# Optimization experiments

Measured on AMD Instinct MI355X. Metric: run time of the kernel, lower is better.

## Reference

```python
import jax, jax.numpy as jnp
import numpy as np

BATCH = 8192
IN_FEATURES = 4096
OUT_FEATURES = 4096
TT_RANK = 8
IN_MODES = (16, 16, 16)
OUT_MODES = (16, 16, 16)


def setup_inputs() -> dict:
    key = jax.random.key(0)
    ks = jax.random.split(key, 5)
    # core std ~ glorot-ish scale for TT factors
    std = 0.05
    x = jax.random.normal(ks[0], (BATCH, IN_FEATURES), dtype=jnp.float32)
    core0 = std * jax.random.normal(ks[1], (1, OUT_MODES[0], IN_MODES[0], TT_RANK), dtype=jnp.float32)
    core1 = std * jax.random.normal(ks[2], (TT_RANK, OUT_MODES[1], IN_MODES[1], TT_RANK), dtype=jnp.float32)
    core2 = std * jax.random.normal(ks[3], (TT_RANK, OUT_MODES[2], IN_MODES[2], 1), dtype=jnp.float32)
    bias = 0.001 * jnp.ones((OUT_FEATURES,), dtype=jnp.float32)
    return {"x": x, "core0": core0, "core1": core1, "core2": core2, "bias": bias}


def _tt_dense_matmul(cores, b):
    """A @ b where A (out_features x in_features) is in TT-matrix format.
    cores[k]: (r_k, o_k, i_k, r_{k+1}), r_0 = r_d = 1. b: (in_features, batch).
    Returns (out_features, batch). Mirrors t3nsor/t3f tt_dense_matmul."""
    in_dims = [c.shape[2] for c in cores]
    ranks = [c.shape[0] for c in cores] + [cores[-1].shape[3]]
    out_features = int(np.prod([c.shape[1] for c in cores]))
    data = b.T                                   # (batch, in_features)
    data = data.reshape(-1, in_dims[-1], 1)      # (batch*prod(i[:-1]), i_last, r_d=1)
    for k in range(len(cores) - 1, -1, -1):
        # core (a=r_k, i=o_k, j=i_k, b=r_{k+1}); data (r, j, b) -> (i, r, a)
        data = jnp.einsum('aijb,rjb->ira', cores[k], data)
        if k > 0:
            data = data.reshape(-1, in_dims[k - 1], ranks[k])
    return data.reshape(out_features, -1)        # (out_features, batch)


def reference(x, core0, core1, core2, bias):
    # forward: tt_dense_matmul(weight_t, x^T)^T + bias
    y = _tt_dense_matmul([core0, core1, core2], x.T)  # (out_features, batch)
    return y.T + bias                                 # (batch, out_features)
```

## Files before the change

kernel.cpp:

```cpp
#include <hip/hip_runtime.h>
#include <cstdint>


typedef __bf16 bf16x8 __attribute__((ext_vector_type(8)));
typedef float f32x4 __attribute__((ext_vector_type(4)));
typedef unsigned short u16;
typedef u16 u16x8 __attribute__((ext_vector_type(8)));

__device__ __forceinline__ u16 f2bf(float f) {
    unsigned u = __builtin_bit_cast(unsigned, f);
    u += 0x7fffu + ((u >> 16) & 1u);
    return (u16)(u >> 16);
}

__global__ void k_cvt(const float* __restrict__ x, u16* __restrict__ xb) {
    long i = (long)blockIdx.x * blockDim.x + threadIdx.x;
    const float4* p = (const float4*)x;
    float4 a = p[2 * i], b = p[2 * i + 1];
    u16x8 o;
    o[0] = f2bf(a.x); o[1] = f2bf(a.y); o[2] = f2bf(a.z); o[3] = f2bf(a.w);
    o[4] = f2bf(b.x); o[5] = f2bf(b.y); o[6] = f2bf(b.z); o[7] = f2bf(b.w);
    ((u16x8*)xb)[i] = o;
}

__global__ void k_c01(const float* __restrict__ c0, const float* __restrict__ c1,
                      float* __restrict__ c01) {
    int idx = blockIdx.x * 256 + threadIdx.x;
    int b2 = idx & 7, i1 = (idx >> 3) & 15, i0 = (idx >> 7) & 15;
    int o1 = (idx >> 11) & 15, o0 = idx >> 15;
    float s = 0.f;
#pragma unroll
    for (int b1 = 0; b1 < 8; ++b1)
        s += c0[(o0 * 16 + i0) * 8 + b1] * c1[((b1 * 16 + o1) * 16 + i1) * 8 + b2];
    c01[idx] = s;
}

__global__ void k_w(const float* __restrict__ c01, const float* __restrict__ c2,
                    u16* __restrict__ wbt) {
    int idx = blockIdx.x * 256 + threadIdx.x;
    int i2h = idx & 1;
    int i1 = (idx >> 1) & 15;
    int i0 = (idx >> 5) & 15;
    int o = idx >> 9;
    int o2 = o & 15, o1 = (o >> 4) & 15, o0 = o >> 8;
    const float* c = &c01[(((o0 * 16 + o1) * 16 + i0) * 16 + i1) * 8];
    float acc[8] = {0, 0, 0, 0, 0, 0, 0, 0};
#pragma unroll
    for (int b2 = 0; b2 < 8; ++b2) {
        float cv = c[b2];
        const float* cc = &c2[(b2 * 16 + o2) * 16 + i2h * 8];
#pragma unroll
        for (int j = 0; j < 8; ++j) acc[j] += cv * cc[j];
    }
    u16x8 ov;
#pragma unroll
    for (int j = 0; j < 8; ++j) ov[j] = f2bf(acc[j]);
    ((u16x8*)wbt)[(long)o * 512 + (i0 * 32 + i1 * 2 + i2h)] = ov;
}

#define BM 256
#define BN 256
#define BK 64
#define TILEU (BM * BK)
#define LDS_BYTES (4 * TILEU * 2)

static_assert(LDS_BYTES == 131072, "lds size");

__device__ __forceinline__ void gload_lds16(const void* g, void* l) {
    __builtin_amdgcn_global_load_lds(
        (const __attribute__((address_space(1))) unsigned*)g,
        (__attribute__((address_space(3))) unsigned*)l, 16, 0, 0);
}

#define VMW(N) asm volatile("s_waitcnt vmcnt(" #N ")" ::: "memory")
#define LGKM0  asm volatile("s_waitcnt lgkmcnt(0)" ::: "memory")
#define BAR()  __builtin_amdgcn_s_barrier()
#define SCHED0 __builtin_amdgcn_sched_barrier(0)

#define READ_A(H, DST, BASE) do { \
    _Pragma("unroll") for (int mi_ = 0; mi_ < 4; ++mi_) { \
        DST[mi_ * 2 + 0] = *(const bf16x8*)&(BASE)[arow + ((H) * 128 + mi_ * 16) * 64 + swz0]; \
        DST[mi_ * 2 + 1] = *(const bf16x8*)&(BASE)[arow + ((H) * 128 + mi_ * 16) * 64 + swz1]; \
    } } while (0)

#define READ_B(G, DST, BASE) do { \
    _Pragma("unroll") for (int ni_ = 0; ni_ < 2; ++ni_) { \
        DST[ni_ * 2 + 0] = *(const bf16x8*)&(BASE)[brow + ((G) * 128 + ni_ * 16) * 64 + swz0]; \
        DST[ni_ * 2 + 1] = *(const bf16x8*)&(BASE)[brow + ((G) * 128 + ni_ * 16) * 64 + swz1]; \
    } } while (0)

#define MFMA16(ASET, BF, H, G) do { \
    __builtin_amdgcn_s_setprio(1); \
    _Pragma("unroll") for (int mi_ = 0; mi_ < 4; ++mi_) \
    _Pragma("unroll") for (int ni_ = 0; ni_ < 2; ++ni_) \
    _Pragma("unroll") for (int kk_ = 0; kk_ < 2; ++kk_) \
        acc[(H) * 4 + mi_][(G) * 2 + ni_] = __builtin_amdgcn_mfma_f32_16x16x32_bf16( \
            ASET[mi_ * 2 + kk_], BF[ni_ * 2 + kk_], acc[(H) * 4 + mi_][(G) * 2 + ni_], 0, 0, 0); \
    __builtin_amdgcn_s_setprio(0); \
} while (0)

#define TILE(BUF, TT, PRE) do { \
    const u16* aT = lds + (BUF) * TILEU; \
    const u16* bT = lds + 2 * TILEU + (BUF) * TILEU; \
    u16* sA = lds + (1 - (BUF)) * TILEU; \
    u16* sB = lds + 2 * TILEU + (1 - (BUF)) * TILEU; \
    const long ko = (long)((TT) + 1) * BK; \
     \
    if (PRE) { gload_lds16(pa[0] + ko, sA + t * 8); \
               gload_lds16(pa[1] + ko, sA + 4096 + t * 8); \
               gload_lds16(pb[0] + ko, sB + t * 8); \
               gload_lds16(pb[1] + ko, sB + 4096 + t * 8); } \
    LGKM0; SCHED0; \
    MFMA16(aA, b0, 0, 0); \
    if (PRE) { VMW(4); } else { VMW(0); } \
    BAR(); \
    READ_B(1, b1, bT); \
     \
    if (PRE) { gload_lds16(pb[2] + ko, sB + 8192 + t * 8); \
               gload_lds16(pb[3] + ko, sB + 12288 + t * 8); \
               gload_lds16(pa[2] + ko, sA + 8192 + t * 8); \
               gload_lds16(pa[3] + ko, sA + 12288 + t * 8); } \
    LGKM0; SCHED0; \
    MFMA16(aA, b1, 0, 1); \
    READ_A(1, aA, aT); \
     \
    if (PRE) { VMW(4); BAR(); } \
    LGKM0; SCHED0; \
    MFMA16(aA, b0, 1, 0); \
    if (PRE) { READ_B(0, b0, sB); } \
     \
    MFMA16(aA, b1, 1, 1); \
    if (PRE) { READ_A(0, aA, sA); } \
} while (0)

__launch_bounds__(512, 2)
__global__ void k_gemm(const u16* __restrict__ A, const u16* __restrict__ B,
                       const float* __restrict__ bias, float* __restrict__ C,
                       int M, int N, int K) {
    extern __shared__ __align__(16) u16 lds[];

    const int wg = blockIdx.x;
    const int swzb = (wg & 7) * 64 + (wg >> 3);
    const int bn = swzb & 15, bm = swzb >> 4;
    const int m0 = bm * BM, n0 = bn * BN;

    const int t = threadIdx.x;
    const int wave = t >> 6, lane = t & 63;
    const int wm = wave >> 2, wn = wave & 3;
    const int lr = lane & 15, quad = lane >> 4;

    const u16 *pa[4], *pb[4];
#pragma unroll
    for (int j = 0; j < 4; ++j) {
        int ci = j * 512 + t;
        int lrow = ci >> 3;
        int c = (ci & 7) ^ (lrow & 7);
        int rA = ((lrow >> 6) & 1) * 128 + (lrow >> 7) * 64 + (lrow & 63);
        int rB = ((lrow >> 5) & 3) * 64 + (lrow >> 7) * 32 + (lrow & 31);
        pa[j] = &A[(long)(m0 + rA) * K + c * 8];
        pb[j] = &B[(long)(n0 + rB) * K + c * 8];
    }

    const int swz0 = ((quad    ) ^ (lr & 7)) * 8;
    const int swz1 = ((quad + 4) ^ (lr & 7)) * 8;
    const int arow = (wm * 64 + lr) * 64;
    const int brow = (wn * 32 + lr) * 64;

    f32x4 acc[8][4];
#pragma unroll
    for (int mi = 0; mi < 8; ++mi)
#pragma unroll
        for (int ni = 0; ni < 4; ++ni) acc[mi][ni] = 0.f;

    bf16x8 aA[8], b0[4], b1[4];

    gload_lds16(pa[0], lds + t * 8);
    gload_lds16(pa[1], lds + 4096 + t * 8);
    gload_lds16(pb[0], lds + 2 * TILEU + t * 8);
    gload_lds16(pb[1], lds + 2 * TILEU + 4096 + t * 8);
    gload_lds16(pb[2], lds + 2 * TILEU + 8192 + t * 8);
    gload_lds16(pb[3], lds + 2 * TILEU + 12288 + t * 8);
    gload_lds16(pa[2], lds + 8192 + t * 8);
    gload_lds16(pa[3], lds + 12288 + t * 8);
    VMW(0); BAR();
    READ_A(0, aA, lds);
    READ_B(0, b0, (lds + 2 * TILEU));

#pragma unroll 1
    for (int tt = 0; tt < 62; tt += 2) {
        TILE(0, tt,     1);
        TILE(1, tt + 1, 1);
    }
    TILE(0, 62, 1);
    TILE(1, 63, 0);

#pragma unroll
    for (int ni = 0; ni < 4; ++ni) {
        int gn = n0 + wn * 64 + ni * 16 + lr;
        float bv = bias[gn];
#pragma unroll
        for (int mi = 0; mi < 8; ++mi) {
            int gm = m0 + wm * 128 + mi * 16 + quad * 4;
#pragma unroll
            for (int r = 0; r < 4; ++r)
                C[(long)(gm + r) * N + gn] = acc[mi][ni][r] + bv;
        }
    }
}

extern "C" void kernel_launch(void* const* d_in, const int* in_sizes, int n_in,
                              void* d_out, int out_size, void* d_ws, size_t ws_size,
                              hipStream_t stream) {
    const float* x = (const float*)d_in[0];
    const float* c0 = (const float*)d_in[1];
    const float* c1 = (const float*)d_in[2];
    const float* c2 = (const float*)d_in[3];
    const float* bias = (const float*)d_in[4];
    float* out = (float*)d_out;

    const int Mb = 8192, Nf = 4096, Kf = 4096;
    char* ws = (char*)d_ws;
    u16* xb = (u16*)ws;
    u16* wbt = (u16*)(ws + 67108864);
    float* c01 = (float*)(ws + 67108864 + 33554432);

    hipFuncSetAttribute(reinterpret_cast<const void*>(k_gemm),
                        hipFuncAttributeMaxDynamicSharedMemorySize, LDS_BYTES);

    k_cvt<<<dim3((Mb * Kf / 8) / 256), 256, 0, stream>>>(x, xb);
    k_c01<<<dim3(2048), 256, 0, stream>>>(c0, c1, c01);
    k_w<<<dim3(8192), 256, 0, stream>>>(c01, c2, wbt);
    k_gemm<<<dim3((Mb / BM) * (Nf / BN)), dim3(512), LDS_BYTES, stream>>>(
        xb, wbt, bias, out, Mb, Nf, Kf);
}
```

Measured before the change: 471.3 us.

## Fuse input conversion and TT weight build into one preprocessing kernel

Merges the fp32-to-bf16 conversion of x, the core0·core1 contraction and the weight expansion into a single kernel. Blocks are split by index between x conversion and weight construction, so the two independent jobs can run at the same time. The c01 intermediate is no longer written to global memory; each thread recomputes its core0·core1 slice in registers. This removes two kernel launches and the c01 round trip. In exchange each weight element does redundant core0·core1 multiply-adds, and the grid is smaller with a fixed amount of work per thread.

```diff
diff --git a/kernel.cpp b/kernel.cpp
--- a/kernel.cpp
+++ b/kernel.cpp
@@ -13,49 +13,54 @@
     return (u16)(u >> 16);
 }
 
-__global__ void k_cvt(const float* __restrict__ x, u16* __restrict__ xb) {
-    long i = (long)blockIdx.x * blockDim.x + threadIdx.x;
-    const float4* p = (const float4*)x;
-    float4 a = p[2 * i], b = p[2 * i + 1];
-    u16x8 o;
-    o[0] = f2bf(a.x); o[1] = f2bf(a.y); o[2] = f2bf(a.z); o[3] = f2bf(a.w);
-    o[4] = f2bf(b.x); o[5] = f2bf(b.y); o[6] = f2bf(b.z); o[7] = f2bf(b.w);
-    ((u16x8*)xb)[i] = o;
-}
-
-__global__ void k_c01(const float* __restrict__ c0, const float* __restrict__ c1,
-                      float* __restrict__ c01) {
-    int idx = blockIdx.x * 256 + threadIdx.x;
-    int b2 = idx & 7, i1 = (idx >> 3) & 15, i0 = (idx >> 7) & 15;
-    int o1 = (idx >> 11) & 15, o0 = idx >> 15;
-    float s = 0.f;
-#pragma unroll
-    for (int b1 = 0; b1 < 8; ++b1)
-        s += c0[(o0 * 16 + i0) * 8 + b1] * c1[((b1 * 16 + o1) * 16 + i1) * 8 + b2];
-    c01[idx] = s;
-}
-
-__global__ void k_w(const float* __restrict__ c01, const float* __restrict__ c2,
-                    u16* __restrict__ wbt) {
-    int idx = blockIdx.x * 256 + threadIdx.x;
-    int i2h = idx & 1;
-    int i1 = (idx >> 1) & 15;
-    int i0 = (idx >> 5) & 15;
-    int o = idx >> 9;
-    int o2 = o & 15, o1 = (o >> 4) & 15, o0 = o >> 8;
-    const float* c = &c01[(((o0 * 16 + o1) * 16 + i0) * 16 + i1) * 8];
-    float acc[8] = {0, 0, 0, 0, 0, 0, 0, 0};
-#pragma unroll
-    for (int b2 = 0; b2 < 8; ++b2) {
-        float cv = c[b2];
-        const float* cc = &c2[(b2 * 16 + o2) * 16 + i2h * 8];
-#pragma unroll
-        for (int j = 0; j < 8; ++j) acc[j] += cv * cc[j];
-    }
-    u16x8 ov;
-#pragma unroll
-    for (int j = 0; j < 8; ++j) ov[j] = f2bf(acc[j]);
-    ((u16x8*)wbt)[(long)o * 512 + (i0 * 32 + i1 * 2 + i2h)] = ov;
+__global__ void k_pre(const float* __restrict__ x, u16* __restrict__ xb,
+                      const float* __restrict__ c0, const float* __restrict__ c1,
+                      const float* __restrict__ c2, u16* __restrict__ wbt) {
+    const int b = blockIdx.x;
+    if (b < 2048) {
+        const float4* p = (const float4*)x;
+        long base = (long)b * 256 + threadIdx.x;
+#pragma unroll
+        for (int it = 0; it < 8; ++it) {
+            long i = base + (long)it * 524288;
+            float4 a = p[2 * i], v = p[2 * i + 1];
+            u16x8 o;
+            o[0] = f2bf(a.x); o[1] = f2bf(a.y); o[2] = f2bf(a.z); o[3] = f2bf(a.w);
+            o[4] = f2bf(v.x); o[5] = f2bf(v.y); o[6] = f2bf(v.z); o[7] = f2bf(v.w);
+            ((u16x8*)xb)[i] = o;
+        }
+    } else {
+        int tb = (b - 2048) * 256 + threadIdx.x;
+#pragma unroll 1
+        for (int it = 0; it < 4; ++it) {
+            int idx = tb + it * 524288;
+            int i2h = idx & 1;
+            int i1 = (idx >> 1) & 15;
+            int i0 = (idx >> 5) & 15;
+            int o = idx >> 9;
+            int o2 = o & 15, o1 = (o >> 4) & 15, o0 = o >> 8;
+            float cb[8] = {0, 0, 0, 0, 0, 0, 0, 0};
+#pragma unroll
+            for (int b1 = 0; b1 < 8; ++b1) {
+                float c0v = c0[(o0 * 16 + i0) * 8 + b1];
+                const float* c1r = &c1[((b1 * 16 + o1) * 16 + i1) * 8];
+#pragma unroll
+                for (int b2 = 0; b2 < 8; ++b2) cb[b2] += c0v * c1r[b2];
+            }
+            float acc[8] = {0, 0, 0, 0, 0, 0, 0, 0};
+#pragma unroll
+            for (int b2 = 0; b2 < 8; ++b2) {
+                float cv = cb[b2];
+                const float* cc = &c2[(b2 * 16 + o2) * 16 + i2h * 8];
+#pragma unroll
+                for (int j = 0; j < 8; ++j) acc[j] += cv * cc[j];
+            }
+            u16x8 ov;
+#pragma unroll
+            for (int j = 0; j < 8; ++j) ov[j] = f2bf(acc[j]);
+            ((u16x8*)wbt)[(long)o * 512 + (i0 * 32 + i1 * 2 + i2h)] = ov;
+        }
+    }
 }
 
 #define BM 256
@@ -222,14 +227,11 @@
     char* ws = (char*)d_ws;
     u16* xb = (u16*)ws;
     u16* wbt = (u16*)(ws + 67108864);
-    float* c01 = (float*)(ws + 67108864 + 33554432);
 
     hipFuncSetAttribute(reinterpret_cast<const void*>(k_gemm),
                         hipFuncAttributeMaxDynamicSharedMemorySize, LDS_BYTES);
 
-    k_cvt<<<dim3((Mb * Kf / 8) / 256), 256, 0, stream>>>(x, xb);
-    k_c01<<<dim3(2048), 256, 0, stream>>>(c0, c1, c01);
-    k_w<<<dim3(8192), 256, 0, stream>>>(c01, c2, wbt);
+    k_pre<<<dim3(4096), 256, 0, stream>>>(x, xb, c0, c1, c2, wbt);
     k_gemm<<<dim3((Mb / BM) * (Nf / BN)), dim3(512), LDS_BYTES, stream>>>(
         xb, wbt, bias, out, Mb, Nf, Kf);
 }
```

New measurement: 470.6 us. About the same (-0.2%).
